# Kernel tuning notes

Measured on AMD Instinct MI355X. Metric: run time of the kernel, lower is better.

The kernel has to match this reference:

```python
import jax, jax.numpy as jnp
import numpy as np

NEG_SLOPE = 0.2  # PyG GATConv default negative_slope


def gat_layer(x, W, a_src, a_dst, bias, src, dst, num_nodes):
    # x: [N, Fin], W: [Fin, H*C], a_src/a_dst: [H, C], bias: [C]
    H, C = a_src.shape
    h = (x @ W).reshape(num_nodes, H, C)                      # [N, H, C]
    alpha_src = jnp.einsum('nhc,hc->nh', h, a_src)            # [N, H]
    alpha_dst = jnp.einsum('nhc,hc->nh', h, a_dst)            # [N, H]
    e = jax.nn.leaky_relu(alpha_src[src] + alpha_dst[dst], NEG_SLOPE)  # [E, H]
    # segment softmax over incoming edges of each destination node
    m = jax.ops.segment_max(e, dst, num_segments=num_nodes)  # [N, H]
    p = jnp.exp(e - m[dst])
    denom = jax.ops.segment_sum(p, dst, num_segments=num_nodes)
    alpha = p / denom[dst]                                    # [E, H]
    out = jax.ops.segment_sum(h[src] * alpha[:, :, None], dst,
                              num_segments=num_nodes)         # [N, H, C]
    return out.mean(axis=1) + bias                            # concat=False -> mean


def setup_inputs() -> dict:
    key = jax.random.key(0)
    ks = jax.random.split(key, 8)
    N, E, F, H = 20000, 640000, 128, 4
    s = 0.1  # weight init scale
    return {
        'x': jax.random.normal(ks[0], (N, F), jnp.float32),
        'W1': jax.random.normal(ks[1], (F, H * F), jnp.float32) * s,
        'a_src1': jax.random.normal(ks[2], (H, F), jnp.float32) * s,
        'a_dst1': jax.random.normal(ks[3], (H, F), jnp.float32) * s,
        'b1': jnp.zeros((F,), jnp.float32),
        'W2': jax.random.normal(ks[4], (F, F), jnp.float32) * s,
        'a_src2': jax.random.normal(ks[5], (1, F), jnp.float32) * s,
        'a_dst2': jax.random.normal(ks[6], (1, F), jnp.float32) * s,
        'b2': jnp.zeros((F,), jnp.float32),
        'edge_index': jax.random.randint(ks[7], (2, E), 0, N, jnp.int32),
    }


def reference(x, W1, a_src1, a_dst1, b1, W2, a_src2, a_dst2, b2, edge_index):
    N = x.shape[0]
    loop = jnp.arange(N, dtype=edge_index.dtype)  # add_self_loops=True (PyG default)
    src = jnp.concatenate([edge_index[0], loop])
    dst = jnp.concatenate([edge_index[1], loop])
    h = jax.nn.elu(gat_layer(x, W1, a_src1, a_dst1, b1, src, dst, N))
    out = jax.nn.elu(gat_layer(h, W2, a_src2, a_dst2, b2, src, dst, N))
    return out
```

## Files before the change

### kernel.cpp

```cpp
#include <hip/hip_runtime.h>
#include <hip/hip_bf16.h>


typedef short v8s __attribute__((ext_vector_type(8)));
typedef float v4f __attribute__((ext_vector_type(4)));
typedef float v2f __attribute__((ext_vector_type(2)));

template <int K> struct IC { static constexpr int value = K; };

constexpr int MAXD = 128;
constexpr int EPB = 4096;
constexpr int BINW = 64;

__device__ __forceinline__ void bf2x(unsigned int u, float& lo, float& hi) {
    union { unsigned int i; float f; } a, b;
    a.i = u << 16;
    b.i = u & 0xffff0000u;
    lo = a.f;
    hi = b.f;
}
__device__ __forceinline__ v2f bf2p(unsigned int u) {
    union { unsigned int i; float f; } a, b;
    a.i = u << 16;
    b.i = u & 0xffff0000u;
    return (v2f){a.f, b.f};
}
__device__ __forceinline__ unsigned short f2bf(float f) {
    union { float f; unsigned int i; } v;
    v.f = f;
    unsigned int lsb = (v.i >> 16) & 1u;
    v.i += 0x7fffu + lsb;
    return (unsigned short)(v.i >> 16);
}
__device__ __forceinline__ unsigned int pack2(float a, float b) {
    return (unsigned int)f2bf(a) | ((unsigned int)f2bf(b) << 16);
}

__device__ __forceinline__ void scan512_incl(unsigned int* a, int tid) {
#pragma unroll
    for (int off = 1; off < 512; off <<= 1) {
        unsigned int v0 = (tid >= off) ? a[tid - off] : 0u;
        unsigned int v1 = a[tid + 256 - off];
        __syncthreads();
        a[tid] += v0;
        a[tid + 256] += v1;
        __syncthreads();
    }
}

__global__ void fused_prep_kernel(const float* __restrict__ x,
                                  const float* __restrict__ W1, const float* __restrict__ W2,
                                  const float* __restrict__ as1v, const float* __restrict__ ad1v,
                                  const float* __restrict__ as2v, const float* __restrict__ ad2v,
                                  unsigned short* __restrict__ xb,
                                  unsigned short* __restrict__ Bt1,
                                  unsigned short* __restrict__ Bt2,
                                  float* __restrict__ wsrc1, float* __restrict__ wdst1,
                                  float* __restrict__ wsrc2, float* __restrict__ wdst2,
                                  float* __restrict__ as2, float* __restrict__ ad2, int N) {
    const int Bcast = (N * 32 + 255) / 256;
    int b = blockIdx.x;
    if (b < Bcast) {
        int i = (b * 256 + threadIdx.x) * 4;
        if (i + 3 < N * 128) {
            float4 v = *(const float4*)&x[i];
            ushort4 o;
            o.x = f2bf(v.x);
            o.y = f2bf(v.y);
            o.z = f2bf(v.z);
            o.w = f2bf(v.w);
            *(ushort4*)&xb[i] = o;
        } else {
            for (; i < N * 128; ++i) xb[i] = f2bf(x[i]);
        }
        return;
    }
    b -= Bcast;
    if (b < 256) {
        int i = b * 256 + threadIdx.x;
        int c = i >> 9;
        int r = i & 511;
        int h = r >> 7, k = r & 127;
        Bt1[i] = f2bf(W1[(size_t)k * 512 + (h << 7) + c] * 0.25f);
        return;
    }
    b -= 256;
    if (b < 64) {
        int i = b * 256 + threadIdx.x;
        int c = i >> 7, k = i & 127;
        Bt2[i] = f2bf(W2[(size_t)k * 128 + c]);
        return;
    }
    b -= 64;
    if (b < 2) {
        int i = b * 256 + threadIdx.x;
        int h = i >> 7, k = i & 127;
        const float* wr = W1 + (size_t)k * 512 + (h << 7);
        const float* as_ = as1v + (h << 7);
        const float* ad_ = ad1v + (h << 7);
        float s1 = 0.f, s2 = 0.f;
        for (int c = 0; c < 128; ++c) {
            float wv = wr[c];
            s1 += wv * as_[c];
            s2 += wv * ad_[c];
        }
        wsrc1[i] = s1;
        wdst1[i] = s2;
        return;
    }
    b -= 2;
    if (b < 1) {
        int k = threadIdx.x;
        if (k < 128) {
            const float* wr = W2 + (size_t)k * 128;
            float s1 = 0.f, s2 = 0.f;
            for (int c = 0; c < 128; ++c) {
                float wv = wr[c];
                s1 += wv * as2v[c];
                s2 += wv * ad2v[c];
            }
            wsrc2[k] = s1;
            wdst2[k] = s2;
        }
        return;
    }
    b -= 1;
    {
        int i = b * 256 + threadIdx.x;
        if (i < N) {
            as2[i] = 0.f;
            ad2[i] = 0.f;
        }
    }
}

__launch_bounds__(256)
__global__ void part_alpha_kernel(const int* __restrict__ src, const int* __restrict__ dst,
                                  int E, unsigned int* __restrict__ binBuf,
                                  unsigned short* __restrict__ boff,
                                  int Bh,
                                  const unsigned int* __restrict__ xrow,
                                  const float* __restrict__ wsrc, const float* __restrict__ wdst,
                                  float* __restrict__ asrc, float* __restrict__ adst, int N) {
    if ((int)blockIdx.x < Bh) {
        __shared__ unsigned int bh[512];
        __shared__ unsigned int stg[EPB];
        const int tid = threadIdx.x;
        bh[tid] = 0u;
        bh[tid + 256] = 0u;
        __syncthreads();
        const int e0 = blockIdx.x * EPB;
        const int ne = min(EPB, E - e0);

        unsigned int pk[16], ps[16];
#pragma unroll
        for (int k = 0; k < 4; ++k) {
            int rel = (k * 256 + tid) * 4;
            if (rel < ne) {
                int4 s4 = *(const int4*)&src[e0 + rel];
                int4 d4 = *(const int4*)&dst[e0 + rel];
                int ss[4] = {s4.x, s4.y, s4.z, s4.w};
                int dd[4] = {d4.x, d4.y, d4.z, d4.w};
#pragma unroll
                for (int j = 0; j < 4; ++j) {
                    unsigned int bin = (unsigned int)dd[j] >> 6;
                    pk[k * 4 + j] = (unsigned int)ss[j] |
                                    (((unsigned int)dd[j] & 63u) << 15) | (bin << 21);
                    ps[k * 4 + j] = atomicAdd(&bh[bin], 1u);
                }
            } else {
#pragma unroll
                for (int j = 0; j < 4; ++j) pk[k * 4 + j] = 0xffffffffu;
            }
        }
        __syncthreads();
        scan512_incl(bh, tid);
#pragma unroll
        for (int k = 0; k < 16; ++k) {
            unsigned int p = pk[k];
            if (p != 0xffffffffu) {
                unsigned int bin = p >> 21;
                unsigned int lo = bin ? bh[bin - 1] : 0u;
                stg[lo + ps[k]] = p;
            }
        }
        __syncthreads();
        unsigned int* out = binBuf + (size_t)blockIdx.x * EPB;
        for (int j = tid; j < ne; j += 256) out[j] = stg[j];
        unsigned short* bo = boff + (size_t)blockIdx.x * 512;
        bo[tid] = (unsigned short)bh[tid];
        bo[tid + 256] = (unsigned short)bh[tid + 256];
        return;
    }
    constexpr int H = 4;
    __shared__ float s_wv[2 * H * 128];
    for (int i = threadIdx.x; i < 2 * H * 128; i += 256)
        s_wv[i] = (i < H * 128) ? wsrc[i] : wdst[i - H * 128];
    __syncthreads();
    const int wid = threadIdx.x >> 6, lane = threadIdx.x & 63;
    const int n = (blockIdx.x - Bh) * 4 + wid;
    if (n >= N) return;
    unsigned int u = xrow[(size_t)n * 64 + lane];
    float f0, f1;
    bf2x(u, f0, f1);
    float s1[H], s2[H];
#pragma unroll
    for (int h = 0; h < H; ++h) {
        float2 ws = *(const float2*)&s_wv[h * 128 + 2 * lane];
        float2 wd = *(const float2*)&s_wv[H * 128 + h * 128 + 2 * lane];
        s1[h] = f0 * ws.x + f1 * ws.y;
        s2[h] = f0 * wd.x + f1 * wd.y;
    }
#pragma unroll
    for (int off = 32; off; off >>= 1)
#pragma unroll
        for (int h = 0; h < H; ++h) {
            s1[h] += __shfl_xor(s1[h], off);
            s2[h] += __shfl_xor(s2[h], off);
        }
    if (lane == 0) {
#pragma unroll
        for (int h = 0; h < H; ++h) {
            asrc[(size_t)n * H + h] = s1[h];
            adst[(size_t)n * H + h] = s2[h];
        }
    }
}

__launch_bounds__(256)
__global__ void csr_build_kernel(const unsigned int* __restrict__ binBuf,
                                 const unsigned short* __restrict__ boff,
                                 unsigned short* __restrict__ slot,
                                 int* __restrict__ cnt, int N, int Bh) {
    __shared__ unsigned int scnt[BINW];
    __shared__ unsigned short sslot[BINW][MAXD];
    const int tid = threadIdx.x;
    const int b = blockIdx.x;
    if (tid < BINW) {
        scnt[tid] = 1u;
        sslot[tid][0] = (unsigned short)(b * BINW + tid);
    }
    __syncthreads();
    for (int k = tid; k < Bh; k += 256) {
        const unsigned short* bo = boff + (size_t)k * 512;
        unsigned int lo = b ? (unsigned int)bo[b - 1] : 0u;
        unsigned int hi = (unsigned int)bo[b];
        const unsigned int* buf = binBuf + (size_t)k * EPB;
        for (unsigned int j = lo; j < hi; ++j) {
            unsigned int p = buf[j];
            int dl = (int)((p >> 15) & 63u);
            unsigned int pos = atomicAdd(&scnt[dl], 1u);
            if (pos < (unsigned int)MAXD) sslot[dl][pos] = (unsigned short)(p & 0x7fffu);
        }
    }
    __syncthreads();
    const int rows = min(BINW, N - b * BINW);
    const int nq = rows * (MAXD / 8);
    uint4* gdst = (uint4*)(slot + (size_t)b * BINW * MAXD);
    const uint4* lsrc = (const uint4*)&sslot[0][0];
    for (int j = tid; j < nq; j += 256) gdst[j] = lsrc[j];
    if (tid < rows) cnt[b * BINW + tid] = (int)min(scnt[tid], (unsigned int)MAXD);
}

template <int H, int NPB>
__launch_bounds__(64 * NPB, 4)
__global__ void gat_gather_kernel(const uint4* __restrict__ xrow4,
                                  const float* __restrict__ asrc,
                                  const float* __restrict__ adst,
                                  const int* __restrict__ cnt,
                                  const unsigned short* __restrict__ slot,
                                  uint4* __restrict__ Sb4,
                                  int N) {
    static_assert(H == 4 || H == 1, "H");
    const int wid = threadIdx.x >> 6, lane = threadIdx.x & 63;
    const int q = lane >> 4, l16 = lane & 15;
    const int n = blockIdx.x * NPB + wid;
    if (n >= N) return;

    __shared__ int s_src_all[NPB][64];
    __shared__ float s_w_all[NPB][64 * H];
    int* s_src = s_src_all[wid];
    float* s_w = s_w_all[wid];

    const int base = n * MAXD;
    const int deg = min(cnt[n], MAXD);

    float adst_n[H];
#pragma unroll
    for (int h = 0; h < H; ++h) adst_n[h] = adst[(size_t)n * H + h];

    float sum_h[H] = {};
    v2f acc[4 * H];
#pragma unroll
    for (int i = 0; i < 4 * H; ++i) acc[i] = (v2f){0.f, 0.f};

    auto do_batch = [&](int j0, auto kc) {
        constexpr int KK = decltype(kc)::value;
        int ss[KK];
        uint4 d[KK];
#pragma unroll
        for (int k = 0; k < KK; ++k) ss[k] = s_src[j0 + k * 4 + q];
#pragma unroll
        for (int k = 0; k < KK; ++k) d[k] = xrow4[(size_t)ss[k] * 16 + l16];
#pragma unroll
        for (int k = 0; k < KK; ++k) {
            v2f f2[4];
            f2[0] = bf2p(d[k].x);
            f2[1] = bf2p(d[k].y);
            f2[2] = bf2p(d[k].z);
            f2[3] = bf2p(d[k].w);
            if constexpr (H == 4) {
                float4 w = *(const float4*)&s_w[(j0 + k * 4 + q) * 4];
                v2f w0 = (v2f){w.x, w.x}, w1 = (v2f){w.y, w.y};
                v2f w2 = (v2f){w.z, w.z}, w3 = (v2f){w.w, w.w};
#pragma unroll
                for (int j = 0; j < 4; ++j) {
                    acc[j] += w0 * f2[j];
                    acc[4 + j] += w1 * f2[j];
                    acc[8 + j] += w2 * f2[j];
                    acc[12 + j] += w3 * f2[j];
                }
            } else {
                float w = s_w[j0 + k * 4 + q];
                v2f w0 = (v2f){w, w};
#pragma unroll
                for (int j = 0; j < 4; ++j) acc[j] += w0 * f2[j];
            }
        }
    };

    for (int i0 = 0; i0 < deg; i0 += 64) {
        const int cntc = min(64, deg - i0);
        {
            const bool valid = lane < cntc;
            int idx = i0 + (valid ? lane : (cntc - 1));
            int s = (int)slot[base + idx];
            s_src[lane] = s;
            if constexpr (H == 4) {
                float4 av = ((const float4*)asrc)[s];
                float ev[4] = {av.x, av.y, av.z, av.w};
#pragma unroll
                for (int hh = 0; hh < 4; ++hh) {
                    float e = ev[hh] + adst_n[hh];
                    e = e > 0.f ? e : 0.2f * e;
                    float wv = valid ? __expf(e) : 0.f;
                    s_w[lane * 4 + hh] = wv;
                    sum_h[hh] += wv;
                }
            } else {
                float e = asrc[s] + adst_n[0];
                e = e > 0.f ? e : 0.2f * e;
                float wv = valid ? __expf(e) : 0.f;
                s_w[lane] = wv;
                sum_h[0] += wv;
            }
        }
        __threadfence_block();

        int j0 = 0;
        for (; j0 + 32 <= cntc; j0 += 32) do_batch(j0, IC<8>{});
        const int rem = cntc - j0;
        if (rem > 0) {
            switch ((rem + 3) >> 2) {
                case 1: do_batch(j0, IC<1>{}); break;
                case 2: do_batch(j0, IC<2>{}); break;
                case 3: do_batch(j0, IC<3>{}); break;
                case 4: do_batch(j0, IC<4>{}); break;
                case 5: do_batch(j0, IC<5>{}); break;
                case 6: do_batch(j0, IC<6>{}); break;
                case 7: do_batch(j0, IC<7>{}); break;
                default: do_batch(j0, IC<8>{}); break;
            }
        }
    }

#pragma unroll
    for (int i = 0; i < 4 * H; ++i) {
        acc[i][0] += __shfl_xor(acc[i][0], 16);
        acc[i][1] += __shfl_xor(acc[i][1], 16);
        acc[i][0] += __shfl_xor(acc[i][0], 32);
        acc[i][1] += __shfl_xor(acc[i][1], 32);
    }
#pragma unroll
    for (int off = 32; off; off >>= 1)
#pragma unroll
        for (int h = 0; h < H; ++h) sum_h[h] += __shfl_xor(sum_h[h], off);

    if constexpr (H == 4) {
#pragma unroll
        for (int h = 0; h < 4; ++h) {
            if (q == h) {
                float rd = 1.0f / sum_h[h];
                uint4 o;
                o.x = pack2(acc[h * 4 + 0][0] * rd, acc[h * 4 + 0][1] * rd);
                o.y = pack2(acc[h * 4 + 1][0] * rd, acc[h * 4 + 1][1] * rd);
                o.z = pack2(acc[h * 4 + 2][0] * rd, acc[h * 4 + 2][1] * rd);
                o.w = pack2(acc[h * 4 + 3][0] * rd, acc[h * 4 + 3][1] * rd);
                Sb4[(size_t)n * 64 + h * 16 + l16] = o;
            }
        }
    } else {
        if (q == 0) {
            float rd = 1.0f / sum_h[0];
            uint4 o;
            o.x = pack2(acc[0][0] * rd, acc[0][1] * rd);
            o.y = pack2(acc[1][0] * rd, acc[1][1] * rd);
            o.z = pack2(acc[2][0] * rd, acc[2][1] * rd);
            o.w = pack2(acc[3][0] * rd, acc[3][1] * rd);
            Sb4[(size_t)n * 16 + l16] = o;
        }
    }
}

__device__ __forceinline__ void store_out(float* p, float v) { *p = v; }
__device__ __forceinline__ void store_out(unsigned short* p, float v) { *p = f2bf(v); }

template <typename OT, bool ELU, bool FUSE_A2>
__launch_bounds__(256)
__global__ void gemm_bias_act_kernel(const unsigned short* __restrict__ A,
                                     const unsigned short* __restrict__ Bt,
                                     const float* __restrict__ bias,
                                     OT* __restrict__ C,
                                     const float* __restrict__ ws2,
                                     const float* __restrict__ wd2,
                                     float* __restrict__ as2, float* __restrict__ ad2,
                                     int M, int Nout, int K) {
    constexpr int BK = 32;
    __shared__ unsigned short As[64][40];
    __shared__ unsigned short Bs[64][40];

    const int tid = threadIdx.x;
    const int w = tid >> 6;
    const int lane = tid & 63;
    const int m16 = lane & 15;
    const int kg = lane >> 4;
    const int m0 = blockIdx.y * 64;
    const int n0 = blockIdx.x * 64;

    v4f acc[4];
#pragma unroll
    for (int i = 0; i < 4; ++i) acc[i] = (v4f){0.f, 0.f, 0.f, 0.f};

    const int srow = tid >> 2;
    const int sseg = tid & 3;
    const int arow_g = min(m0 + srow, M - 1);
    const unsigned short* Ap = &A[(size_t)arow_g * K + sseg * 8];
    const unsigned short* Bp = &Bt[(size_t)(n0 + srow) * K + sseg * 8];

    for (int k0 = 0; k0 < K; k0 += BK) {
        uint4 av = *(const uint4*)(Ap + k0);
        uint4 bv = *(const uint4*)(Bp + k0);
        __syncthreads();
        *(uint4*)&As[srow][sseg * 8] = av;
        *(uint4*)&Bs[srow][sseg * 8] = bv;
        __syncthreads();
        v8s a = *(const v8s*)&As[w * 16 + m16][kg * 8];
#pragma unroll
        for (int i = 0; i < 4; ++i) {
            v8s b = *(const v8s*)&Bs[i * 16 + m16][kg * 8];
            acc[i] = __builtin_amdgcn_mfma_f32_16x16x32_bf16(a, b, acc[i], 0, 0, 0);
        }
    }

    float pr_s[4] = {}, pr_d[4] = {};
#pragma unroll
    for (int i = 0; i < 4; ++i) {
        const int col = n0 + i * 16 + m16;
        const float bv = bias[col];
        float w2s = 0.f, w2d = 0.f;
        if constexpr (FUSE_A2) {
            w2s = ws2[col];
            w2d = wd2[col];
        }
#pragma unroll
        for (int r = 0; r < 4; ++r) {
            int row = m0 + w * 16 + kg * 4 + r;
            if (row < M) {
                float val = acc[i][r] + bv;
                if constexpr (ELU) val = val > 0.f ? val : (__expf(val) - 1.0f);
                store_out(&C[(size_t)row * Nout + col], val);
                if constexpr (FUSE_A2) {
                    pr_s[r] += val * w2s;
                    pr_d[r] += val * w2d;
                }
            }
        }
    }
    if constexpr (FUSE_A2) {
#pragma unroll
        for (int off = 1; off < 16; off <<= 1)
#pragma unroll
            for (int r = 0; r < 4; ++r) {
                pr_s[r] += __shfl_xor(pr_s[r], off);
                pr_d[r] += __shfl_xor(pr_d[r], off);
            }
        if (m16 == 0) {
#pragma unroll
            for (int r = 0; r < 4; ++r) {
                int row = m0 + w * 16 + kg * 4 + r;
                if (row < M) {
                    atomicAdd(&as2[row], pr_s[r]);
                    atomicAdd(&ad2[row], pr_d[r]);
                }
            }
        }
    }
}


extern "C" void kernel_launch(void* const* d_in, const int* in_sizes, int n_in,
                              void* d_out, int out_size, void* d_ws, size_t ws_size,
                              hipStream_t stream) {
    const float* x = (const float*)d_in[0];
    const float* W1 = (const float*)d_in[1];
    const float* a_src1 = (const float*)d_in[2];
    const float* a_dst1 = (const float*)d_in[3];
    const float* b1 = (const float*)d_in[4];
    const float* W2 = (const float*)d_in[5];
    const float* a_src2 = (const float*)d_in[6];
    const float* a_dst2 = (const float*)d_in[7];
    const float* b2 = (const float*)d_in[8];
    const int* edge = (const int*)d_in[9];
    float* out = (float*)d_out;

    constexpr int F = 128, H = 4;
    const int N = in_sizes[0] / F;
    const int E = in_sizes[9] / 2;
    const int Bh = (E + EPB - 1) / EPB;

    char* ws = (char*)d_ws;
    size_t o = 0;
    auto take = [&](size_t bytes) {
        char* p = ws + o;
        o = (o + bytes + 255) & ~(size_t)255;
        return p;
    };
    int* cnt = (int*)take((size_t)N * 4);
    unsigned short* slot = (unsigned short*)take((size_t)N * MAXD * 2);
    unsigned int* binBuf = (unsigned int*)take((size_t)Bh * EPB * 4);
    unsigned short* boff = (unsigned short*)take((size_t)Bh * 512 * 2);
    unsigned short* xb = (unsigned short*)take((size_t)N * F * 2);
    unsigned short* Bt1 = (unsigned short*)take((size_t)F * H * F * 2);
    unsigned short* Bt2 = (unsigned short*)take((size_t)F * F * 2);
    float* wsrc1 = (float*)take((size_t)H * F * 4);
    float* wdst1 = (float*)take((size_t)H * F * 4);
    float* wsrc2 = (float*)take((size_t)F * 4);
    float* wdst2 = (float*)take((size_t)F * 4);
    float* as1 = (float*)take((size_t)N * H * 4);
    float* ad1 = (float*)take((size_t)N * H * 4);
    unsigned short* Sb1 = (unsigned short*)take((size_t)N * H * F * 2);
    unsigned short* h2b = (unsigned short*)take((size_t)N * F * 2);
    float* as2 = (float*)take((size_t)N * 4);
    float* ad2 = (float*)take((size_t)N * 4);
    unsigned short* S2b = (unsigned short*)take((size_t)N * F * 2);
    (void)ws_size;

    const int* esrc = edge;
    const int* edst = edge + E;

    const int Bcast = (N * 32 + 255) / 256;
    const int Bzero = (N + 255) / 256;
    hipLaunchKernelGGL(fused_prep_kernel, dim3(Bcast + 256 + 64 + 2 + 1 + Bzero), dim3(256), 0,
                       stream, x, W1, W2, a_src1, a_dst1, a_src2, a_dst2, xb, Bt1, Bt2, wsrc1,
                       wdst1, wsrc2, wdst2, as2, ad2, N);

    const int Balpha = (N + 3) / 4;
    hipLaunchKernelGGL(part_alpha_kernel, dim3(Bh + Balpha), dim3(256), 0, stream, esrc, edst,
                       E, binBuf, boff, Bh, (const unsigned int*)xb, wsrc1, wdst1, as1, ad1, N);

    const int NB = (N + BINW - 1) / BINW;
    hipLaunchKernelGGL(csr_build_kernel, dim3(NB), dim3(256), 0, stream, binBuf, boff, slot,
                       cnt, N, Bh);

    hipLaunchKernelGGL((gat_gather_kernel<H, 4>), dim3((N + 3) / 4), dim3(256), 0, stream,
                       (const uint4*)xb, as1, ad1, cnt, slot, (uint4*)Sb1, N);
    hipLaunchKernelGGL((gemm_bias_act_kernel<unsigned short, true, true>),
                       dim3(F / 64, (N + 63) / 64), dim3(256), 0, stream, Sb1, Bt1, b1, h2b,
                       wsrc2, wdst2, as2, ad2, N, F, H * F);

    hipLaunchKernelGGL((gat_gather_kernel<1, 4>), dim3((N + 3) / 4), dim3(256), 0, stream,
                       (const uint4*)h2b, as2, ad2, cnt, slot, (uint4*)S2b, N);
    hipLaunchKernelGGL((gemm_bias_act_kernel<float, true, false>), dim3(F / 64, (N + 63) / 64),
                       dim3(256), 0, stream, S2b, Bt2, b2, out, nullptr, nullptr, nullptr,
                       nullptr, N, F, F);
}
```

Before: 190.6 us.

## Regroup edge partition into prep kernel and CSR build with alpha kernel

```diff
diff --git a/kernel.cpp b/kernel.cpp
--- a/kernel.cpp
+++ b/kernel.cpp
@@ -48,18 +48,74 @@
     }
 }
 
-__global__ void fused_prep_kernel(const float* __restrict__ x,
-                                  const float* __restrict__ W1, const float* __restrict__ W2,
-                                  const float* __restrict__ as1v, const float* __restrict__ ad1v,
-                                  const float* __restrict__ as2v, const float* __restrict__ ad2v,
-                                  unsigned short* __restrict__ xb,
-                                  unsigned short* __restrict__ Bt1,
-                                  unsigned short* __restrict__ Bt2,
-                                  float* __restrict__ wsrc1, float* __restrict__ wdst1,
-                                  float* __restrict__ wsrc2, float* __restrict__ wdst2,
-                                  float* __restrict__ as2, float* __restrict__ ad2, int N) {
+__launch_bounds__(256)
+__global__ void prep_part_kernel(const int* __restrict__ src, const int* __restrict__ dst,
+                                 int E, unsigned int* __restrict__ binBuf,
+                                 unsigned short* __restrict__ boff,
+                                 int Bh,
+                                 const float* __restrict__ x,
+                                 const float* __restrict__ W1, const float* __restrict__ W2,
+                                 const float* __restrict__ as1v, const float* __restrict__ ad1v,
+                                 const float* __restrict__ as2v, const float* __restrict__ ad2v,
+                                 unsigned short* __restrict__ xb,
+                                 unsigned short* __restrict__ Bt1,
+                                 unsigned short* __restrict__ Bt2,
+                                 float* __restrict__ wsrc1, float* __restrict__ wdst1,
+                                 float* __restrict__ wsrc2, float* __restrict__ wdst2,
+                                 float* __restrict__ as2, float* __restrict__ ad2, int N) {
+    int b = blockIdx.x;
+    if (b < Bh) {
+        __shared__ unsigned int bh[512];
+        __shared__ unsigned int stg[EPB];
+        const int tid = threadIdx.x;
+        bh[tid] = 0u;
+        bh[tid + 256] = 0u;
+        __syncthreads();
+        const int e0 = b * EPB;
+        const int ne = min(EPB, E - e0);
+
+        unsigned int pk[16], ps[16];
+#pragma unroll
+        for (int k = 0; k < 4; ++k) {
+            int rel = (k * 256 + tid) * 4;
+            if (rel < ne) {
+                int4 s4 = *(const int4*)&src[e0 + rel];
+                int4 d4 = *(const int4*)&dst[e0 + rel];
+                int ss[4] = {s4.x, s4.y, s4.z, s4.w};
+                int dd[4] = {d4.x, d4.y, d4.z, d4.w};
+#pragma unroll
+                for (int j = 0; j < 4; ++j) {
+                    unsigned int bin = (unsigned int)dd[j] >> 6;
+                    pk[k * 4 + j] = (unsigned int)ss[j] |
+                                    (((unsigned int)dd[j] & 63u) << 15) | (bin << 21);
+                    ps[k * 4 + j] = atomicAdd(&bh[bin], 1u);
+                }
+            } else {
+#pragma unroll
+                for (int j = 0; j < 4; ++j) pk[k * 4 + j] = 0xffffffffu;
+            }
+        }
+        __syncthreads();
+        scan512_incl(bh, tid);
+#pragma unroll
+        for (int k = 0; k < 16; ++k) {
+            unsigned int p = pk[k];
+            if (p != 0xffffffffu) {
+                unsigned int bin = p >> 21;
+                unsigned int lo = bin ? bh[bin - 1] : 0u;
+                stg[lo + ps[k]] = p;
+            }
+        }
+        __syncthreads();
+        unsigned int* out = binBuf + (size_t)b * EPB;
+        for (int j = tid; j < ne; j += 256) out[j] = stg[j];
+        unsigned short* bo = boff + (size_t)b * 512;
+        bo[tid] = (unsigned short)bh[tid];
+        bo[tid + 256] = (unsigned short)bh[tid + 256];
+        return;
+    }
+    b -= Bh;
     const int Bcast = (N * 32 + 255) / 256;
-    int b = blockIdx.x;
     if (b < Bcast) {
         int i = (b * 256 + threadIdx.x) * 4;
         if (i + 3 < N * 128) {
@@ -135,61 +191,43 @@
 }
 
 __launch_bounds__(256)
-__global__ void part_alpha_kernel(const int* __restrict__ src, const int* __restrict__ dst,
-                                  int E, unsigned int* __restrict__ binBuf,
-                                  unsigned short* __restrict__ boff,
-                                  int Bh,
-                                  const unsigned int* __restrict__ xrow,
-                                  const float* __restrict__ wsrc, const float* __restrict__ wdst,
-                                  float* __restrict__ asrc, float* __restrict__ adst, int N) {
-    if ((int)blockIdx.x < Bh) {
-        __shared__ unsigned int bh[512];
-        __shared__ unsigned int stg[EPB];
+__global__ void build_alpha_kernel(const unsigned int* __restrict__ binBuf,
+                                   const unsigned short* __restrict__ boff,
+                                   unsigned short* __restrict__ slot,
+                                   int* __restrict__ cnt, int N, int Bh, int NB,
+                                   const unsigned int* __restrict__ xrow,
+                                   const float* __restrict__ wsrc,
+                                   const float* __restrict__ wdst,
+                                   float* __restrict__ asrc, float* __restrict__ adst) {
+    if ((int)blockIdx.x < NB) {
+        __shared__ unsigned int scnt[BINW];
+        __shared__ unsigned short sslot[BINW][MAXD];
         const int tid = threadIdx.x;
-        bh[tid] = 0u;
-        bh[tid + 256] = 0u;
-        __syncthreads();
-        const int e0 = blockIdx.x * EPB;
-        const int ne = min(EPB, E - e0);
-
-        unsigned int pk[16], ps[16];
-#pragma unroll
-        for (int k = 0; k < 4; ++k) {
-            int rel = (k * 256 + tid) * 4;
-            if (rel < ne) {
-                int4 s4 = *(const int4*)&src[e0 + rel];
-                int4 d4 = *(const int4*)&dst[e0 + rel];
-                int ss[4] = {s4.x, s4.y, s4.z, s4.w};
-                int dd[4] = {d4.x, d4.y, d4.z, d4.w};
-#pragma unroll
-                for (int j = 0; j < 4; ++j) {
-                    unsigned int bin = (unsigned int)dd[j] >> 6;
-                    pk[k * 4 + j] = (unsigned int)ss[j] |
-                                    (((unsigned int)dd[j] & 63u) << 15) | (bin << 21);
-                    ps[k * 4 + j] = atomicAdd(&bh[bin], 1u);
-                }
-            } else {
-#pragma unroll
-                for (int j = 0; j < 4; ++j) pk[k * 4 + j] = 0xffffffffu;
-            }
-        }
-        __syncthreads();
-        scan512_incl(bh, tid);
-#pragma unroll
-        for (int k = 0; k < 16; ++k) {
-            unsigned int p = pk[k];
-            if (p != 0xffffffffu) {
-                unsigned int bin = p >> 21;
-                unsigned int lo = bin ? bh[bin - 1] : 0u;
-                stg[lo + ps[k]] = p;
-            }
-        }
-        __syncthreads();
-        unsigned int* out = binBuf + (size_t)blockIdx.x * EPB;
-        for (int j = tid; j < ne; j += 256) out[j] = stg[j];
-        unsigned short* bo = boff + (size_t)blockIdx.x * 512;
-        bo[tid] = (unsigned short)bh[tid];
-        bo[tid + 256] = (unsigned short)bh[tid + 256];
+        const int b = blockIdx.x;
+        if (tid < BINW) {
+            scnt[tid] = 1u;
+            sslot[tid][0] = (unsigned short)(b * BINW + tid);
+        }
+        __syncthreads();
+        for (int k = tid; k < Bh; k += 256) {
+            const unsigned short* bo = boff + (size_t)k * 512;
+            unsigned int lo = b ? (unsigned int)bo[b - 1] : 0u;
+            unsigned int hi = (unsigned int)bo[b];
+            const unsigned int* buf = binBuf + (size_t)k * EPB;
+            for (unsigned int j = lo; j < hi; ++j) {
+                unsigned int p = buf[j];
+                int dl = (int)((p >> 15) & 63u);
+                unsigned int pos = atomicAdd(&scnt[dl], 1u);
+                if (pos < (unsigned int)MAXD) sslot[dl][pos] = (unsigned short)(p & 0x7fffu);
+            }
+        }
+        __syncthreads();
+        const int rows = min(BINW, N - b * BINW);
+        const int nq = rows * (MAXD / 8);
+        uint4* gdst = (uint4*)(slot + (size_t)b * BINW * MAXD);
+        const uint4* lsrc = (const uint4*)&sslot[0][0];
+        for (int j = tid; j < nq; j += 256) gdst[j] = lsrc[j];
+        if (tid < rows) cnt[b * BINW + tid] = (int)min(scnt[tid], (unsigned int)MAXD);
         return;
     }
     constexpr int H = 4;
@@ -198,7 +236,7 @@
         s_wv[i] = (i < H * 128) ? wsrc[i] : wdst[i - H * 128];
     __syncthreads();
     const int wid = threadIdx.x >> 6, lane = threadIdx.x & 63;
-    const int n = (blockIdx.x - Bh) * 4 + wid;
+    const int n = (blockIdx.x - NB) * 4 + wid;
     if (n >= N) return;
     unsigned int u = xrow[(size_t)n * 64 + lane];
     float f0, f1;
@@ -225,41 +263,6 @@
             adst[(size_t)n * H + h] = s2[h];
         }
     }
-}
-
-__launch_bounds__(256)
-__global__ void csr_build_kernel(const unsigned int* __restrict__ binBuf,
-                                 const unsigned short* __restrict__ boff,
-                                 unsigned short* __restrict__ slot,
-                                 int* __restrict__ cnt, int N, int Bh) {
-    __shared__ unsigned int scnt[BINW];
-    __shared__ unsigned short sslot[BINW][MAXD];
-    const int tid = threadIdx.x;
-    const int b = blockIdx.x;
-    if (tid < BINW) {
-        scnt[tid] = 1u;
-        sslot[tid][0] = (unsigned short)(b * BINW + tid);
-    }
-    __syncthreads();
-    for (int k = tid; k < Bh; k += 256) {
-        const unsigned short* bo = boff + (size_t)k * 512;
-        unsigned int lo = b ? (unsigned int)bo[b - 1] : 0u;
-        unsigned int hi = (unsigned int)bo[b];
-        const unsigned int* buf = binBuf + (size_t)k * EPB;
-        for (unsigned int j = lo; j < hi; ++j) {
-            unsigned int p = buf[j];
-            int dl = (int)((p >> 15) & 63u);
-            unsigned int pos = atomicAdd(&scnt[dl], 1u);
-            if (pos < (unsigned int)MAXD) sslot[dl][pos] = (unsigned short)(p & 0x7fffu);
-        }
-    }
-    __syncthreads();
-    const int rows = min(BINW, N - b * BINW);
-    const int nq = rows * (MAXD / 8);
-    uint4* gdst = (uint4*)(slot + (size_t)b * BINW * MAXD);
-    const uint4* lsrc = (const uint4*)&sslot[0][0];
-    for (int j = tid; j < nq; j += 256) gdst[j] = lsrc[j];
-    if (tid < rows) cnt[b * BINW + tid] = (int)min(scnt[tid], (unsigned int)MAXD);
 }
 
 template <int H, int NPB>
@@ -527,6 +530,7 @@
     const int N = in_sizes[0] / F;
     const int E = in_sizes[9] / 2;
     const int Bh = (E + EPB - 1) / EPB;
+    const int NB = (N + BINW - 1) / BINW;
 
     char* ws = (char*)d_ws;
     size_t o = 0;
@@ -560,17 +564,14 @@
 
     const int Bcast = (N * 32 + 255) / 256;
     const int Bzero = (N + 255) / 256;
-    hipLaunchKernelGGL(fused_prep_kernel, dim3(Bcast + 256 + 64 + 2 + 1 + Bzero), dim3(256), 0,
-                       stream, x, W1, W2, a_src1, a_dst1, a_src2, a_dst2, xb, Bt1, Bt2, wsrc1,
-                       wdst1, wsrc2, wdst2, as2, ad2, N);
+    hipLaunchKernelGGL(prep_part_kernel, dim3(Bh + Bcast + 256 + 64 + 2 + 1 + Bzero), dim3(256),
+                       0, stream, esrc, edst, E, binBuf, boff, Bh, x, W1, W2, a_src1, a_dst1,
+                       a_src2, a_dst2, xb, Bt1, Bt2, wsrc1, wdst1, wsrc2, wdst2, as2, ad2, N);
 
     const int Balpha = (N + 3) / 4;
-    hipLaunchKernelGGL(part_alpha_kernel, dim3(Bh + Balpha), dim3(256), 0, stream, esrc, edst,
-                       E, binBuf, boff, Bh, (const unsigned int*)xb, wsrc1, wdst1, as1, ad1, N);
-
-    const int NB = (N + BINW - 1) / BINW;
-    hipLaunchKernelGGL(csr_build_kernel, dim3(NB), dim3(256), 0, stream, binBuf, boff, slot,
-                       cnt, N, Bh);
+    hipLaunchKernelGGL(build_alpha_kernel, dim3(NB + Balpha), dim3(256), 0, stream, binBuf,
+                       boff, slot, cnt, N, Bh, NB, (const unsigned int*)xb, wsrc1, wdst1, as1,
+                       ad1);
 
     hipLaunchKernelGGL((gat_gather_kernel<H, 4>), dim3((N + 3) / 4), dim3(256), 0, stream,
                        (const uint4*)xb, as1, ad1, cnt, slot, (uint4*)Sb1, N);
```

Measured after the change: 180.0 us (median of 2 runs). 5.6% less time.
